# Kernel optimization log

Hardware: AMD Instinct MI355X
Metric: run time of the kernel (lower is better)

## Reference

```python
import jax, jax.numpy as jnp
import numpy as np

WS = 7
C = 384
NH = 12
HD = C // NH
HID = 4 * C


def layernorm(x, g, b, eps=1e-5):
    m = jnp.mean(x, axis=-1, keepdims=True)
    v = jnp.mean((x - m) ** 2, axis=-1, keepdims=True)
    return (x - m) * jax.lax.rsqrt(v + eps) * g + b


def setup_inputs() -> dict:
    key = jax.random.key(0)
    ks = jax.random.split(key, 12)
    s = 0.02
    return {
        "tokens": jax.random.normal(ks[0], (2, 8, 56 * 56, C), jnp.float32),
        "in_proj_w": jax.random.normal(ks[1], (3 * C, C), jnp.float32) * s,
        "in_proj_b": jnp.zeros((3 * C,), jnp.float32),
        "out_w": jax.random.normal(ks[2], (C, C), jnp.float32) * s,
        "out_b": jnp.zeros((C,), jnp.float32),
        "ln1_g": jnp.ones((C,), jnp.float32),
        "ln1_b": jnp.zeros((C,), jnp.float32),
        "w1": jax.random.normal(ks[3], (HID, C), jnp.float32) * s,
        "b1": jnp.zeros((HID,), jnp.float32),
        "w2": jax.random.normal(ks[4], (C, HID), jnp.float32) * s,
        "b2": jnp.zeros((C,), jnp.float32),
        "ln2_g": jnp.ones((C,), jnp.float32),
        "ln2_b": jnp.zeros((C,), jnp.float32),
        "h": 56,
        "w": 56,
    }


def _block(tokens, in_proj_w, in_proj_b, out_w, out_b, ln1_g, ln1_b, w1, b1, w2, b2, ln2_g, ln2_b, h, w):
    b, t, _, c = tokens.shape
    orig_h, orig_w = h, w
    x = tokens.reshape(b, t, h, w, c)
    pad_h = (-h) % WS
    pad_w = (-w) % WS
    if pad_h > 0 or pad_w > 0:
        x = jnp.pad(x, ((0, 0), (0, 0), (0, pad_h), (0, pad_w), (0, 0)))
        h, w = h + pad_h, w + pad_w
    nh, nw = h // WS, w // WS
    # window partition -> [N, 49, C]
    x = x.reshape(b, t, nh, WS, nw, WS, c).transpose(0, 1, 2, 4, 3, 5, 6)
    win = x.reshape(b * t * nh * nw, WS * WS, c)
    # MHA (torch nn.MultiheadAttention semantics)
    a = layernorm(win, ln1_g, ln1_b)
    qkv = a @ in_proj_w.T + in_proj_b  # [N, 49, 3C]
    q, k, v = jnp.split(qkv, 3, axis=-1)
    n, s, _ = q.shape
    q = q.reshape(n, s, NH, HD).transpose(0, 2, 1, 3)
    k = k.reshape(n, s, NH, HD).transpose(0, 2, 1, 3)
    v = v.reshape(n, s, NH, HD).transpose(0, 2, 1, 3)
    scores = jnp.einsum("nhqd,nhkd->nhqk", q, k) / jnp.sqrt(jnp.asarray(HD, q.dtype))
    p = jax.nn.softmax(scores, axis=-1)
    o = jnp.einsum("nhqk,nhkd->nhqd", p, v).transpose(0, 2, 1, 3).reshape(n, s, c)
    win = win + (o @ out_w.T + out_b)
    # MLP
    m = layernorm(win, ln2_g, ln2_b)
    m = jax.nn.gelu(m @ w1.T + b1, approximate=False) @ w2.T + b2
    win = win + m
    # window reverse
    x = win.reshape(b, t, nh, nw, WS, WS, c).transpose(0, 1, 2, 4, 3, 5, 6).reshape(b, t, h, w, c)
    x = x[:, :, :orig_h, :orig_w, :]
    return x.reshape(b, t, orig_h * orig_w, c)


def reference(tokens, in_proj_w, in_proj_b, out_w, out_b, ln1_g, ln1_b, w1, b1, w2, b2, ln2_g, ln2_b, h, w):
    return _block(tokens, in_proj_w, in_proj_b, out_w, out_b, ln1_g, ln1_b, w1, b1, w2, b2, ln2_g, ln2_b, h, w)
```

## Files before the change

kernel.cpp:

```cpp
#include <hip/hip_runtime.h>
#include <hip/hip_bf16.h>
#include <math.h>

using short8 = __attribute__((ext_vector_type(8))) short;
using f32x4  = __attribute__((ext_vector_type(4))) float;

#define MFMA_B16(A,B,C) __builtin_amdgcn_mfma_f32_16x16x32_bf16((A),(B),(C),0,0,0)

#define ALN_STR 392
#define Q2_OFF  38416
#define QK_STR  72
#define K2_OFF  45472
#define VT_OFF  52528
#define VT_STR  72
#define OH_OFF  61744
#define OH_STR  72
#define HID0_OFF 38416
#define HID1_OFF 55824
#define HID_STR 136
#define SMEM_BYTES 80896

__device__ __forceinline__ unsigned f2bf(float x) {
  unsigned u = __float_as_uint(x);
  return (u + 0x7fffu + ((u >> 16) & 1u)) >> 16;
}

template<bool WBF>
__device__ __forceinline__ short8 loadW(const void* base, int tile, int K8, int kcb,
                                        int l, int row, int ldk, int k0) {
  if constexpr (WBF) {
    return *(const short8*)((const unsigned short*)base +
                            (((size_t)(tile * K8 + kcb)) << 7) + l * 8);
  } else {
    const float* p = (const float*)base + (size_t)row * ldk + k0;
    float4 x = *(const float4*)p;
    float4 y = *(const float4*)(p + 4);
    short8 r;
    r[0]=(short)f2bf(x.x); r[1]=(short)f2bf(x.y); r[2]=(short)f2bf(x.z); r[3]=(short)f2bf(x.w);
    r[4]=(short)f2bf(y.x); r[5]=(short)f2bf(y.y); r[6]=(short)f2bf(y.z); r[7]=(short)f2bf(y.w);
    return r;
  }
}

__global__ void cvt_pack(const float* __restrict__ src, unsigned short* __restrict__ dst,
                         int K, int n) {
  int K8 = K >> 3;
  int i = blockIdx.x * blockDim.x + threadIdx.x;
  if (i >= n) return;
  int e = i & 7;
  int idx = i >> 3;
  int r = idx & 15; idx >>= 4;
  int kc = idx % K8, ci = idx / K8;
  dst[i] = (unsigned short)f2bf(src[(size_t)(ci * 16 + r) * K + kc * 8 + e]);
}

template<bool WBF>
__global__ __launch_bounds__(512, 4)
void swin_mfma(const float* __restrict__ tokens,
               const void* __restrict__ ipw,  const float* __restrict__ ipb,
               const void* __restrict__ outw, const float* __restrict__ outb,
               const float* __restrict__ ln1g, const float* __restrict__ ln1b,
               const void* __restrict__ w1,   const float* __restrict__ b1,
               const void* __restrict__ w2,   const float* __restrict__ b2,
               const float* __restrict__ ln2g, const float* __restrict__ ln2b,
               float* __restrict__ out)
{
  extern __shared__ char smem[];
  unsigned short* aln  = (unsigned short*)smem;
  unsigned short* q2   = (unsigned short*)(smem + Q2_OFF);
  unsigned short* k2   = (unsigned short*)(smem + K2_OFF);
  unsigned short* vT2  = (unsigned short*)(smem + VT_OFF);
  unsigned short* oh   = (unsigned short*)(smem + OH_OFF);
  unsigned short* hid0 = (unsigned short*)(smem + HID0_OFF);
  unsigned short* hid1 = (unsigned short*)(smem + HID1_OFF);

  const int tid = threadIdx.x;
  const int l  = tid & 63, wv = tid >> 6;
  const int cl = l & 15,  kg = l >> 4;
  const int wid = blockIdx.x;
  const int iw = wid & 7, ih = (wid >> 3) & 7, bt = wid >> 6;

  auto gidx = [&](int r, int c) -> size_t {
    int wi = r / 7, wj = r - wi * 7;
    return ((size_t)bt * 3136 + (size_t)((ih*7 + wi) * 56 + iw*7 + wj)) * 384 + c;
  };

  auto ln_pass = [&](const float* src, const float* gw, const float* gb) {
    int grp = tid >> 3, lj = tid & 7;
    if (grp < 49) {
      size_t base = gidx(grp, 0);
      float4 xv[12];
      float sx = 0.f, sxx = 0.f;
      #pragma unroll
      for (int k = 0; k < 12; ++k) {
        xv[k] = *(const float4*)&src[base + (lj + 8*k) * 4];
        sx  += xv[k].x + xv[k].y + xv[k].z + xv[k].w;
        sxx += xv[k].x*xv[k].x + xv[k].y*xv[k].y + xv[k].z*xv[k].z + xv[k].w*xv[k].w;
      }
      #pragma unroll
      for (int d = 1; d < 8; d <<= 1) { sx += __shfl_xor(sx, d, 8); sxx += __shfl_xor(sxx, d, 8); }
      float mean = sx * (1.f/384.f);
      float rs = rsqrtf(sxx * (1.f/384.f) - mean*mean + 1e-5f);
      unsigned short* arow = aln + grp * ALN_STR;
      #pragma unroll
      for (int k = 0; k < 12; ++k) {
        int c = (lj + 8*k) * 4;
        float4 gv = *(const float4*)&gw[c];
        float4 bv = *(const float4*)&gb[c];
        unsigned u0 = f2bf((xv[k].x-mean)*rs*gv.x + bv.x) | (f2bf((xv[k].y-mean)*rs*gv.y + bv.y) << 16);
        unsigned u1 = f2bf((xv[k].z-mean)*rs*gv.z + bv.z) | (f2bf((xv[k].w-mean)*rs*gv.w + bv.w) << 16);
        *(uint2*)&arow[c] = make_uint2(u0, u1);
      }
    }
  };

  const int ri0 = wv & 3, chalf = wv >> 2;
  const int arow0 = (cl + 16 * ri0) * ALN_STR;

  auto qkv = [&](int pr) {
    #pragma unroll
    for (int half = 0; half < 2; ++half) {
      int cia[3], tilea[3], growa[3];
      #pragma unroll
      for (int j = 0; j < 3; ++j) {
        int ci = chalf + 2 * (half * 3 + j);
        int part = ci >> 2, wt = ci & 3;
        cia[j] = ci;
        tilea[j] = part * 24 + pr * 4 + wt;
        growa[j] = part * 384 + pr * 64 + wt * 16 + cl;
      }
      f32x4 d0{0,0,0,0}, d1{0,0,0,0}, d2{0,0,0,0};
      #pragma unroll
      for (int kt = 0; kt < 12; ++kt) {
        int k0 = kt * 32 + kg * 8;
        short8 a = *(const short8*)&aln[arow0 + k0];
        short8 b0 = loadW<WBF>(ipw, tilea[0], 48, kt*4, l, growa[0], 384, k0);
        short8 b1 = loadW<WBF>(ipw, tilea[1], 48, kt*4, l, growa[1], 384, k0);
        short8 b2 = loadW<WBF>(ipw, tilea[2], 48, kt*4, l, growa[2], 384, k0);
        d0 = MFMA_B16(a, b0, d0);
        d1 = MFMA_B16(a, b1, d1);
        d2 = MFMA_B16(a, b2, d2);
      }
      #pragma unroll
      for (int j = 0; j < 3; ++j) {
        f32x4 dd = (j == 0) ? d0 : (j == 1) ? d1 : d2;
        int part = cia[j] >> 2;
        int within = (cia[j] & 3) * 16 + cl;
        float bias = ipb[growa[j]];
        float scl = (part == 0) ? 0.17677669529663687f : 1.f;
        #pragma unroll
        for (int rg = 0; rg < 4; ++rg) {
          int row = kg * 4 + rg + 16 * ri0;
          if (row < 49) {
            unsigned short bv = (unsigned short)f2bf((dd[rg] + bias) * scl);
            if      (part == 0) q2[row * QK_STR + within] = bv;
            else if (part == 1) k2[row * QK_STR + within] = bv;
            else                vT2[within * VT_STR + row] = bv;
          }
        }
      }
    }
  };

  for (int i = tid; i < (64*VT_STR)/2; i += 512) ((unsigned*)(smem + VT_OFF))[i] = 0u;
  ln_pass(tokens, ln1g, ln1b);
  __syncthreads();

  f32x4 opacc[3][4];
  #pragma unroll
  for (int a = 0; a < 3; ++a)
    #pragma unroll
    for (int b = 0; b < 4; ++b) opacc[a][b] = f32x4{0.f,0.f,0.f,0.f};

  qkv(0);
  __syncthreads();

  const int hl = wv & 1, qci = wv >> 1;

  for (int pr = 0; pr < 6; ++pr) {
    {
      short8 bq = *(const short8*)&q2[(16*qci + cl) * QK_STR + hl*32 + kg*8];
      f32x4 dsc[4];
      #pragma unroll
      for (int kri = 0; kri < 4; ++kri) {
        short8 ak = *(const short8*)&k2[(16*kri + cl) * QK_STR + hl*32 + kg*8];
        f32x4 z{0.f,0.f,0.f,0.f};
        dsc[kri] = MFMA_B16(ak, bq, z);
      }
      float ev[4][4];
      float mx = -1e30f;
      #pragma unroll
      for (int kri = 0; kri < 4; ++kri)
        #pragma unroll
        for (int r = 0; r < 4; ++r) {
          int kidx = 16*kri + 4*kg + r;
          float v = (kidx < 49) ? dsc[kri][r] : -1e30f;
          ev[kri][r] = v;
          mx = fmaxf(mx, v);
        }
      mx = fmaxf(mx, __shfl_xor(mx, 16));
      mx = fmaxf(mx, __shfl_xor(mx, 32));
      float sum = 0.f;
      #pragma unroll
      for (int kri = 0; kri < 4; ++kri)
        #pragma unroll
        for (int r = 0; r < 4; ++r) {
          float e = __expf(ev[kri][r] - mx);
          ev[kri][r] = e; sum += e;
        }
      sum += __shfl_xor(sum, 16);
      sum += __shfl_xor(sum, 32);
      float inv = 1.f / sum;
      unsigned pk[4][2];
      #pragma unroll
      for (int kri = 0; kri < 4; ++kri) {
        pk[kri][0] = f2bf(ev[kri][0]*inv) | (f2bf(ev[kri][1]*inv) << 16);
        pk[kri][1] = f2bf(ev[kri][2]*inv) | (f2bf(ev[kri][3]*inv) << 16);
      }
      f32x4 dot0{0.f,0.f,0.f,0.f}, dot1{0.f,0.f,0.f,0.f};
      const int sA = cl + 32 * (kg & 1);
      const bool hi = (kg >> 1) & 1;
      #pragma unroll
      for (int kt = 0; kt < 2; ++kt) {
        unsigned x0 = (unsigned)__shfl((int)pk[2*kt][0],   sA);
        unsigned x1 = (unsigned)__shfl((int)pk[2*kt][1],   sA);
        unsigned x2 = (unsigned)__shfl((int)pk[2*kt][0],   sA + 16);
        unsigned x3 = (unsigned)__shfl((int)pk[2*kt][1],   sA + 16);
        unsigned y0 = (unsigned)__shfl((int)pk[2*kt+1][0], sA);
        unsigned y1 = (unsigned)__shfl((int)pk[2*kt+1][1], sA);
        unsigned y2 = (unsigned)__shfl((int)pk[2*kt+1][0], sA + 16);
        unsigned y3 = (unsigned)__shfl((int)pk[2*kt+1][1], sA + 16);
        uint4 bu = make_uint4(hi ? y0 : x0, hi ? y1 : x1, hi ? y2 : x2, hi ? y3 : x3);
        short8 bfrag = *(short8*)&bu;
        short8 a0 = *(const short8*)&vT2[(hl*32 +  0 + cl) * VT_STR + kt*32 + kg*8];
        short8 a1 = *(const short8*)&vT2[(hl*32 + 16 + cl) * VT_STR + kt*32 + kg*8];
        dot0 = MFMA_B16(a0, bfrag, dot0);
        dot1 = MFMA_B16(a1, bfrag, dot1);
      }
      int q = 16*qci + cl;
      if (q < 49) {
        int base = q * OH_STR + hl*32 + kg*4;
        *(unsigned*)&oh[base     ] = f2bf(dot0[0]) | (f2bf(dot0[1]) << 16);
        *(unsigned*)&oh[base +  2] = f2bf(dot0[2]) | (f2bf(dot0[3]) << 16);
        *(unsigned*)&oh[base + 16] = f2bf(dot1[0]) | (f2bf(dot1[1]) << 16);
        *(unsigned*)&oh[base + 18] = f2bf(dot1[2]) | (f2bf(dot1[3]) << 16);
      }
    }
    __syncthreads();

    {
      short8 ao[4][2];
      #pragma unroll
      for (int ri = 0; ri < 4; ++ri)
        #pragma unroll
        for (int kt = 0; kt < 2; ++kt)
          ao[ri][kt] = *(const short8*)&oh[(cl + 16*ri) * OH_STR + kt*32 + kg*8];
      #pragma unroll
      for (int cii = 0; cii < 3; ++cii) {
        #pragma unroll
        for (int kt = 0; kt < 2; ++kt) {
          short8 bw = loadW<WBF>(outw, wv*3 + cii, 48, pr*8 + kt*4, l,
                                 (wv*3 + cii)*16 + cl, 384, pr*64 + kt*32 + kg*8);
          opacc[cii][0] = MFMA_B16(ao[0][kt], bw, opacc[cii][0]);
          opacc[cii][1] = MFMA_B16(ao[1][kt], bw, opacc[cii][1]);
          opacc[cii][2] = MFMA_B16(ao[2][kt], bw, opacc[cii][2]);
          opacc[cii][3] = MFMA_B16(ao[3][kt], bw, opacc[cii][3]);
        }
      }
      if (pr < 5) qkv(pr + 1);
    }
    __syncthreads();
  }

  #pragma unroll
  for (int cii = 0; cii < 3; ++cii) {
    int col = (wv*3 + cii) * 16 + cl;
    float ob = outb[col];
    #pragma unroll
    for (int ri = 0; ri < 4; ++ri) {
      #pragma unroll
      for (int rg = 0; rg < 4; ++rg) {
        int row = kg*4 + rg + 16*ri;
        if (row < 49) {
          size_t g = gidx(row, col);
          out[g] = tokens[g] + opacc[cii][ri][rg] + ob;
        }
      }
    }
  }
  __syncthreads();

  ln_pass(out, ln2g, ln2b);
  __syncthreads();

  f32x4 macc[3][4];
  #pragma unroll
  for (int a = 0; a < 3; ++a)
    #pragma unroll
    for (int b = 0; b < 4; ++b) macc[a][b] = f32x4{0.f,0.f,0.f,0.f};

  auto mlp1 = [&](int cc, unsigned short* hb) {
    int tile = cc * 8 + wv;
    int n = cc * 128 + wv * 16 + cl;
    f32x4 e0{0,0,0,0}, e1{0,0,0,0}, e2{0,0,0,0}, e3{0,0,0,0};
    #pragma unroll
    for (int kt = 0; kt < 12; ++kt) {
      int k0 = kt * 32 + kg * 8;
      short8 bw = loadW<WBF>(w1, tile, 48, kt*4, l, n, 384, k0);
      short8 a0 = *(const short8*)&aln[(cl     ) * ALN_STR + k0];
      short8 a1 = *(const short8*)&aln[(cl + 16) * ALN_STR + k0];
      short8 a2 = *(const short8*)&aln[(cl + 32) * ALN_STR + k0];
      short8 a3 = *(const short8*)&aln[(cl + 48) * ALN_STR + k0];
      e0 = MFMA_B16(a0, bw, e0);
      e1 = MFMA_B16(a1, bw, e1);
      e2 = MFMA_B16(a2, bw, e2);
      e3 = MFMA_B16(a3, bw, e3);
    }
    float bb = b1[n];
    #pragma unroll
    for (int ri = 0; ri < 4; ++ri) {
      f32x4 ee = (ri == 0) ? e0 : (ri == 1) ? e1 : (ri == 2) ? e2 : e3;
      #pragma unroll
      for (int rg = 0; rg < 4; ++rg) {
        int row = kg*4 + rg + 16*ri;
        if (row < 49) {
          float x = ee[rg] + bb;
          float gl = 0.5f * x * (1.f + erff(x * 0.70710678118654752f));
          hb[row * HID_STR + wv*16 + cl] = (unsigned short)f2bf(gl);
        }
      }
    }
  };
  auto mlp2 = [&](int cc, const unsigned short* hb) {
    #pragma unroll
    for (int kt = 0; kt < 4; ++kt) {
      int k0 = kt * 32 + kg * 8;
      short8 h0_ = *(const short8*)&hb[(cl     ) * HID_STR + k0];
      short8 h1_ = *(const short8*)&hb[(cl + 16) * HID_STR + k0];
      short8 h2_ = *(const short8*)&hb[(cl + 32) * HID_STR + k0];
      short8 h3_ = *(const short8*)&hb[(cl + 48) * HID_STR + k0];
      #pragma unroll
      for (int cii = 0; cii < 3; ++cii) {
        short8 bw = loadW<WBF>(w2, wv*3 + cii, 192, cc*16 + kt*4, l,
                               (wv*3 + cii)*16 + cl, 1536, cc*128 + k0);
        macc[cii][0] = MFMA_B16(h0_, bw, macc[cii][0]);
        macc[cii][1] = MFMA_B16(h1_, bw, macc[cii][1]);
        macc[cii][2] = MFMA_B16(h2_, bw, macc[cii][2]);
        macc[cii][3] = MFMA_B16(h3_, bw, macc[cii][3]);
      }
    }
  };

  mlp1(0, hid0);
  __syncthreads();
  for (int cc = 1; cc < 12; ++cc) {
    mlp2(cc - 1, ((cc - 1) & 1) ? hid1 : hid0);
    mlp1(cc, (cc & 1) ? hid1 : hid0);
    __syncthreads();
  }
  mlp2(11, hid1);

  #pragma unroll
  for (int cii = 0; cii < 3; ++cii) {
    int col = (wv*3 + cii) * 16 + cl;
    float bb2 = b2[col];
    #pragma unroll
    for (int ri = 0; ri < 4; ++ri) {
      #pragma unroll
      for (int rg = 0; rg < 4; ++rg) {
        int row = kg*4 + rg + 16*ri;
        if (row < 49) {
          size_t g = gidx(row, col);
          out[g] = out[g] + macc[cii][ri][rg] + bb2;
        }
      }
    }
  }
}

#define WS_IPW  0
#define WS_OUTW 442368
#define WS_W1   589824
#define WS_W2   1179648
#define WS_TOT  1769472

extern "C" void kernel_launch(void* const* d_in, const int* in_sizes, int n_in,
                              void* d_out, int out_size, void* d_ws, size_t ws_size,
                              hipStream_t stream) {
  (void)in_sizes; (void)n_in; (void)out_size;
  const float* tokens = (const float*)d_in[0];
  const float* ipw  = (const float*)d_in[1];
  const float* ipb  = (const float*)d_in[2];
  const float* outw = (const float*)d_in[3];
  const float* outb = (const float*)d_in[4];
  const float* ln1g = (const float*)d_in[5];
  const float* ln1b = (const float*)d_in[6];
  const float* w1   = (const float*)d_in[7];
  const float* b1   = (const float*)d_in[8];
  const float* w2   = (const float*)d_in[9];
  const float* b2   = (const float*)d_in[10];
  const float* ln2g = (const float*)d_in[11];
  const float* ln2b = (const float*)d_in[12];
  float* out = (float*)d_out;

  bool wbf = (ws_size >= (size_t)WS_TOT * 2);
  if (wbf) {
    unsigned short* wsp = (unsigned short*)d_ws;
    hipLaunchKernelGGL(cvt_pack, dim3((442368+511)/512), dim3(512), 0, stream, ipw,  wsp + WS_IPW,  384,  442368);
    hipLaunchKernelGGL(cvt_pack, dim3((147456+511)/512), dim3(512), 0, stream, outw, wsp + WS_OUTW, 384,  147456);
    hipLaunchKernelGGL(cvt_pack, dim3((589824+511)/512), dim3(512), 0, stream, w1,   wsp + WS_W1,   384,  589824);
    hipLaunchKernelGGL(cvt_pack, dim3((589824+511)/512), dim3(512), 0, stream, w2,   wsp + WS_W2,   1536, 589824);
    (void)hipFuncSetAttribute((const void*)swin_mfma<true>,
                              hipFuncAttributeMaxDynamicSharedMemorySize, SMEM_BYTES);
    hipLaunchKernelGGL((swin_mfma<true>), dim3(1024), dim3(512), SMEM_BYTES, stream,
                       tokens, (const void*)(wsp + WS_IPW), ipb,
                       (const void*)(wsp + WS_OUTW), outb, ln1g, ln1b,
                       (const void*)(wsp + WS_W1), b1, (const void*)(wsp + WS_W2), b2,
                       ln2g, ln2b, out);
  } else {
    (void)hipFuncSetAttribute((const void*)swin_mfma<false>,
                              hipFuncAttributeMaxDynamicSharedMemorySize, SMEM_BYTES);
    hipLaunchKernelGGL((swin_mfma<false>), dim3(1024), dim3(512), SMEM_BYTES, stream,
                       tokens, (const void*)ipw, ipb, (const void*)outw, outb, ln1g, ln1b,
                       (const void*)w1, b1, (const void*)w2, b2, ln2g, ln2b, out);
  }
}
```

Baseline: 475.2 us.

## Process two windows per 1024-thread block, prefetch weights, use tanh-form GELU

Each block now holds two 49-token windows with 1024 threads, each with its own LDS region, so the block count is halved. The QKV, MLP1 and MLP2 loops now load the next k-step's weight fragments into registers before issuing the current MFMAs, to hide global-load latency. The exact erf GELU is replaced by a tanh approximation written as x*sigmoid, which is cheaper but changes numerics slightly. Using 146 KB of LDS per block caps residency at one block per CU, and the extra prefetch registers may spill.

```diff
diff --git a/kernel.cpp b/kernel.cpp
--- a/kernel.cpp
+++ b/kernel.cpp
@@ -8,21 +8,21 @@
 #define MFMA_B16(A,B,C) __builtin_amdgcn_mfma_f32_16x16x32_bf16((A),(B),(C),0,0,0)
 
 #define ALN_STR 392
-#define Q2_OFF  38416
+#define ALN_SZ  38416
+#define POOL    76832
+#define PS      34816
 #define QK_STR  72
-#define K2_OFF  45472
-#define VT_OFF  52528
 #define VT_STR  72
-#define OH_OFF  61744
 #define OH_STR  72
-#define HID0_OFF 38416
-#define HID1_OFF 55824
 #define HID_STR 136
-#define SMEM_BYTES 80896
-
-__device__ __forceinline__ unsigned f2bf(float x) {
+#define SMEM_BYTES 146464
+
+__device__ __forceinline__ unsigned short f2bfu(float x) {
   unsigned u = __float_as_uint(x);
-  return (u + 0x7fffu + ((u >> 16) & 1u)) >> 16;
+  return (unsigned short)((u + 0x7fffu + ((u >> 16) & 1u)) >> 16);
+}
+__device__ __forceinline__ unsigned pk2(float a, float b) {
+  return (unsigned)f2bfu(a) | ((unsigned)f2bfu(b) << 16);
 }
 
 template<bool WBF>
@@ -36,8 +36,8 @@
     float4 x = *(const float4*)p;
     float4 y = *(const float4*)(p + 4);
     short8 r;
-    r[0]=(short)f2bf(x.x); r[1]=(short)f2bf(x.y); r[2]=(short)f2bf(x.z); r[3]=(short)f2bf(x.w);
-    r[4]=(short)f2bf(y.x); r[5]=(short)f2bf(y.y); r[6]=(short)f2bf(y.z); r[7]=(short)f2bf(y.w);
+    r[0]=(short)f2bfu(x.x); r[1]=(short)f2bfu(x.y); r[2]=(short)f2bfu(x.z); r[3]=(short)f2bfu(x.w);
+    r[4]=(short)f2bfu(y.x); r[5]=(short)f2bfu(y.y); r[6]=(short)f2bfu(y.z); r[7]=(short)f2bfu(y.w);
     return r;
   }
 }
@@ -51,11 +51,11 @@
   int idx = i >> 3;
   int r = idx & 15; idx >>= 4;
   int kc = idx % K8, ci = idx / K8;
-  dst[i] = (unsigned short)f2bf(src[(size_t)(ci * 16 + r) * K + kc * 8 + e]);
+  dst[i] = f2bfu(src[(size_t)(ci * 16 + r) * K + kc * 8 + e]);
 }
 
 template<bool WBF>
-__global__ __launch_bounds__(512, 4)
+__global__ __launch_bounds__(1024, 4)
 void swin_mfma(const float* __restrict__ tokens,
                const void* __restrict__ ipw,  const float* __restrict__ ipb,
                const void* __restrict__ outw, const float* __restrict__ outb,
@@ -66,19 +66,22 @@
                float* __restrict__ out)
 {
   extern __shared__ char smem[];
-  unsigned short* aln  = (unsigned short*)smem;
-  unsigned short* q2   = (unsigned short*)(smem + Q2_OFF);
-  unsigned short* k2   = (unsigned short*)(smem + K2_OFF);
-  unsigned short* vT2  = (unsigned short*)(smem + VT_OFF);
-  unsigned short* oh   = (unsigned short*)(smem + OH_OFF);
-  unsigned short* hid0 = (unsigned short*)(smem + HID0_OFF);
-  unsigned short* hid1 = (unsigned short*)(smem + HID1_OFF);
-
   const int tid = threadIdx.x;
-  const int l  = tid & 63, wv = tid >> 6;
-  const int cl = l & 15,  kg = l >> 4;
-  const int wid = blockIdx.x;
+  const int win = tid >> 9;
+  const int wv  = (tid >> 6) & 7;
+  const int l   = tid & 63;
+  const int cl  = l & 15, kg = l >> 4;
+  const int wid = blockIdx.x * 2 + win;
   const int iw = wid & 7, ih = (wid >> 3) & 7, bt = wid >> 6;
+
+  unsigned short* aln = (unsigned short*)(smem + win * ALN_SZ);
+  char* pool = smem + POOL + win * PS;
+  unsigned short* q2   = (unsigned short*)(pool);
+  unsigned short* k2   = (unsigned short*)(pool + 7056);
+  unsigned short* vT2  = (unsigned short*)(pool + 14112);
+  unsigned short* oh   = (unsigned short*)(pool + 23328);
+  unsigned short* hid0 = (unsigned short*)(pool);
+  unsigned short* hid1 = (unsigned short*)(pool + 17408);
 
   auto gidx = [&](int r, int c) -> size_t {
     int wi = r / 7, wj = r - wi * 7;
@@ -86,9 +89,9 @@
   };
 
   auto ln_pass = [&](const float* src, const float* gw, const float* gb) {
-    int grp = tid >> 3, lj = tid & 7;
-    if (grp < 49) {
-      size_t base = gidx(grp, 0);
+    int row = (tid >> 3) & 63, lj = tid & 7;
+    if (row < 49) {
+      size_t base = gidx(row, 0);
       float4 xv[12];
       float sx = 0.f, sxx = 0.f;
       #pragma unroll
@@ -101,14 +104,14 @@
       for (int d = 1; d < 8; d <<= 1) { sx += __shfl_xor(sx, d, 8); sxx += __shfl_xor(sxx, d, 8); }
       float mean = sx * (1.f/384.f);
       float rs = rsqrtf(sxx * (1.f/384.f) - mean*mean + 1e-5f);
-      unsigned short* arow = aln + grp * ALN_STR;
+      unsigned short* arow = aln + row * ALN_STR;
       #pragma unroll
       for (int k = 0; k < 12; ++k) {
         int c = (lj + 8*k) * 4;
         float4 gv = *(const float4*)&gw[c];
         float4 bv = *(const float4*)&gb[c];
-        unsigned u0 = f2bf((xv[k].x-mean)*rs*gv.x + bv.x) | (f2bf((xv[k].y-mean)*rs*gv.y + bv.y) << 16);
-        unsigned u1 = f2bf((xv[k].z-mean)*rs*gv.z + bv.z) | (f2bf((xv[k].w-mean)*rs*gv.w + bv.w) << 16);
+        unsigned u0 = pk2((xv[k].x-mean)*rs*gv.x + bv.x, (xv[k].y-mean)*rs*gv.y + bv.y);
+        unsigned u1 = pk2((xv[k].z-mean)*rs*gv.z + bv.z, (xv[k].w-mean)*rs*gv.w + bv.w);
         *(uint2*)&arow[c] = make_uint2(u0, u1);
       }
     }
@@ -120,49 +123,56 @@
   auto qkv = [&](int pr) {
     #pragma unroll
     for (int half = 0; half < 2; ++half) {
-      int cia[3], tilea[3], growa[3];
+      int tilea[3], growa[3], parta[3], wta[3];
       #pragma unroll
       for (int j = 0; j < 3; ++j) {
         int ci = chalf + 2 * (half * 3 + j);
-        int part = ci >> 2, wt = ci & 3;
-        cia[j] = ci;
-        tilea[j] = part * 24 + pr * 4 + wt;
-        growa[j] = part * 384 + pr * 64 + wt * 16 + cl;
+        parta[j] = ci >> 2; wta[j] = ci & 3;
+        tilea[j] = parta[j] * 24 + pr * 4 + wta[j];
+        growa[j] = parta[j] * 384 + pr * 64 + wta[j] * 16 + cl;
       }
       f32x4 d0{0,0,0,0}, d1{0,0,0,0}, d2{0,0,0,0};
+      short8 a_c  = *(const short8*)&aln[arow0 + kg*8];
+      short8 b0_c = loadW<WBF>(ipw, tilea[0], 48, 0, l, growa[0], 384, kg*8);
+      short8 b1_c = loadW<WBF>(ipw, tilea[1], 48, 0, l, growa[1], 384, kg*8);
+      short8 b2_c = loadW<WBF>(ipw, tilea[2], 48, 0, l, growa[2], 384, kg*8);
       #pragma unroll
       for (int kt = 0; kt < 12; ++kt) {
-        int k0 = kt * 32 + kg * 8;
-        short8 a = *(const short8*)&aln[arow0 + k0];
-        short8 b0 = loadW<WBF>(ipw, tilea[0], 48, kt*4, l, growa[0], 384, k0);
-        short8 b1 = loadW<WBF>(ipw, tilea[1], 48, kt*4, l, growa[1], 384, k0);
-        short8 b2 = loadW<WBF>(ipw, tilea[2], 48, kt*4, l, growa[2], 384, k0);
-        d0 = MFMA_B16(a, b0, d0);
-        d1 = MFMA_B16(a, b1, d1);
-        d2 = MFMA_B16(a, b2, d2);
+        short8 a_n, b0_n, b1_n, b2_n;
+        if (kt < 11) {
+          int k1 = (kt+1)*32 + kg*8;
+          a_n  = *(const short8*)&aln[arow0 + k1];
+          b0_n = loadW<WBF>(ipw, tilea[0], 48, (kt+1)*4, l, growa[0], 384, k1);
+          b1_n = loadW<WBF>(ipw, tilea[1], 48, (kt+1)*4, l, growa[1], 384, k1);
+          b2_n = loadW<WBF>(ipw, tilea[2], 48, (kt+1)*4, l, growa[2], 384, k1);
+        }
+        d0 = MFMA_B16(a_c, b0_c, d0);
+        d1 = MFMA_B16(a_c, b1_c, d1);
+        d2 = MFMA_B16(a_c, b2_c, d2);
+        a_c = a_n; b0_c = b0_n; b1_c = b1_n; b2_c = b2_n;
       }
       #pragma unroll
       for (int j = 0; j < 3; ++j) {
         f32x4 dd = (j == 0) ? d0 : (j == 1) ? d1 : d2;
-        int part = cia[j] >> 2;
-        int within = (cia[j] & 3) * 16 + cl;
+        int within = wta[j] * 16 + cl;
         float bias = ipb[growa[j]];
-        float scl = (part == 0) ? 0.17677669529663687f : 1.f;
+        float scl = (parta[j] == 0) ? 0.17677669529663687f : 1.f;
         #pragma unroll
         for (int rg = 0; rg < 4; ++rg) {
           int row = kg * 4 + rg + 16 * ri0;
           if (row < 49) {
-            unsigned short bv = (unsigned short)f2bf((dd[rg] + bias) * scl);
-            if      (part == 0) q2[row * QK_STR + within] = bv;
-            else if (part == 1) k2[row * QK_STR + within] = bv;
-            else                vT2[within * VT_STR + row] = bv;
+            unsigned short bv = f2bfu((dd[rg] + bias) * scl);
+            if      (parta[j] == 0) q2[row * QK_STR + within] = bv;
+            else if (parta[j] == 1) k2[row * QK_STR + within] = bv;
+            else                    vT2[within * VT_STR + row] = bv;
           }
         }
       }
     }
   };
 
-  for (int i = tid; i < (64*VT_STR)/2; i += 512) ((unsigned*)(smem + VT_OFF))[i] = 0u;
+  for (int i = (tid & 511); i < (64*VT_STR)/2; i += 512)
+    ((unsigned*)(pool + 14112))[i] = 0u;
   ln_pass(tokens, ln1g, ln1b);
   __syncthreads();
 
@@ -214,8 +224,8 @@
       unsigned pk[4][2];
       #pragma unroll
       for (int kri = 0; kri < 4; ++kri) {
-        pk[kri][0] = f2bf(ev[kri][0]*inv) | (f2bf(ev[kri][1]*inv) << 16);
-        pk[kri][1] = f2bf(ev[kri][2]*inv) | (f2bf(ev[kri][3]*inv) << 16);
+        pk[kri][0] = pk2(ev[kri][0]*inv, ev[kri][1]*inv);
+        pk[kri][1] = pk2(ev[kri][2]*inv, ev[kri][3]*inv);
       }
       f32x4 dot0{0.f,0.f,0.f,0.f}, dot1{0.f,0.f,0.f,0.f};
       const int sA = cl + 32 * (kg & 1);
@@ -240,10 +250,10 @@
       int q = 16*qci + cl;
       if (q < 49) {
         int base = q * OH_STR + hl*32 + kg*4;
-        *(unsigned*)&oh[base     ] = f2bf(dot0[0]) | (f2bf(dot0[1]) << 16);
-        *(unsigned*)&oh[base +  2] = f2bf(dot0[2]) | (f2bf(dot0[3]) << 16);
-        *(unsigned*)&oh[base + 16] = f2bf(dot1[0]) | (f2bf(dot1[1]) << 16);
-        *(unsigned*)&oh[base + 18] = f2bf(dot1[2]) | (f2bf(dot1[3]) << 16);
+        *(unsigned*)&oh[base     ] = pk2(dot0[0], dot0[1]);
+        *(unsigned*)&oh[base +  2] = pk2(dot0[2], dot0[3]);
+        *(unsigned*)&oh[base + 16] = pk2(dot1[0], dot1[1]);
+        *(unsigned*)&oh[base + 18] = pk2(dot1[2], dot1[3]);
       }
     }
     __syncthreads();
@@ -303,18 +313,22 @@
     int tile = cc * 8 + wv;
     int n = cc * 128 + wv * 16 + cl;
     f32x4 e0{0,0,0,0}, e1{0,0,0,0}, e2{0,0,0,0}, e3{0,0,0,0};
+    short8 bw_c = loadW<WBF>(w1, tile, 48, 0, l, n, 384, kg*8);
     #pragma unroll
     for (int kt = 0; kt < 12; ++kt) {
+      short8 bw_n;
+      if (kt < 11)
+        bw_n = loadW<WBF>(w1, tile, 48, (kt+1)*4, l, n, 384, (kt+1)*32 + kg*8);
       int k0 = kt * 32 + kg * 8;
-      short8 bw = loadW<WBF>(w1, tile, 48, kt*4, l, n, 384, k0);
       short8 a0 = *(const short8*)&aln[(cl     ) * ALN_STR + k0];
       short8 a1 = *(const short8*)&aln[(cl + 16) * ALN_STR + k0];
       short8 a2 = *(const short8*)&aln[(cl + 32) * ALN_STR + k0];
       short8 a3 = *(const short8*)&aln[(cl + 48) * ALN_STR + k0];
-      e0 = MFMA_B16(a0, bw, e0);
-      e1 = MFMA_B16(a1, bw, e1);
-      e2 = MFMA_B16(a2, bw, e2);
-      e3 = MFMA_B16(a3, bw, e3);
+      e0 = MFMA_B16(a0, bw_c, e0);
+      e1 = MFMA_B16(a1, bw_c, e1);
+      e2 = MFMA_B16(a2, bw_c, e2);
+      e3 = MFMA_B16(a3, bw_c, e3);
+      bw_c = bw_n;
     }
     float bb = b1[n];
     #pragma unroll
@@ -325,29 +339,46 @@
         int row = kg*4 + rg + 16*ri;
         if (row < 49) {
           float x = ee[rg] + bb;
-          float gl = 0.5f * x * (1.f + erff(x * 0.70710678118654752f));
-          hb[row * HID_STR + wv*16 + cl] = (unsigned short)f2bf(gl);
+          float t2 = 0.044715f * x * x;
+          float arg = __builtin_fmaf(t2, x, x);
+          float e = __expf(1.5957691216f * arg);
+          float gl = x * (e / (e + 1.f));
+          hb[row * HID_STR + wv*16 + cl] = f2bfu(gl);
         }
       }
     }
   };
   auto mlp2 = [&](int cc, const unsigned short* hb) {
+    short8 c0_c = loadW<WBF>(w2, wv*3+0, 192, cc*16, l, (wv*3+0)*16+cl, 1536, cc*128 + kg*8);
+    short8 c1_c = loadW<WBF>(w2, wv*3+1, 192, cc*16, l, (wv*3+1)*16+cl, 1536, cc*128 + kg*8);
+    short8 c2_c = loadW<WBF>(w2, wv*3+2, 192, cc*16, l, (wv*3+2)*16+cl, 1536, cc*128 + kg*8);
     #pragma unroll
     for (int kt = 0; kt < 4; ++kt) {
+      short8 c0_n, c1_n, c2_n;
+      if (kt < 3) {
+        int kcb = cc*16 + (kt+1)*4, k1 = cc*128 + (kt+1)*32 + kg*8;
+        c0_n = loadW<WBF>(w2, wv*3+0, 192, kcb, l, (wv*3+0)*16+cl, 1536, k1);
+        c1_n = loadW<WBF>(w2, wv*3+1, 192, kcb, l, (wv*3+1)*16+cl, 1536, k1);
+        c2_n = loadW<WBF>(w2, wv*3+2, 192, kcb, l, (wv*3+2)*16+cl, 1536, k1);
+      }
       int k0 = kt * 32 + kg * 8;
       short8 h0_ = *(const short8*)&hb[(cl     ) * HID_STR + k0];
       short8 h1_ = *(const short8*)&hb[(cl + 16) * HID_STR + k0];
       short8 h2_ = *(const short8*)&hb[(cl + 32) * HID_STR + k0];
       short8 h3_ = *(const short8*)&hb[(cl + 48) * HID_STR + k0];
-      #pragma unroll
-      for (int cii = 0; cii < 3; ++cii) {
-        short8 bw = loadW<WBF>(w2, wv*3 + cii, 192, cc*16 + kt*4, l,
-                               (wv*3 + cii)*16 + cl, 1536, cc*128 + k0);
-        macc[cii][0] = MFMA_B16(h0_, bw, macc[cii][0]);
-        macc[cii][1] = MFMA_B16(h1_, bw, macc[cii][1]);
-        macc[cii][2] = MFMA_B16(h2_, bw, macc[cii][2]);
-        macc[cii][3] = MFMA_B16(h3_, bw, macc[cii][3]);
-      }
+      macc[0][0] = MFMA_B16(h0_, c0_c, macc[0][0]);
+      macc[0][1] = MFMA_B16(h1_, c0_c, macc[0][1]);
+      macc[0][2] = MFMA_B16(h2_, c0_c, macc[0][2]);
+      macc[0][3] = MFMA_B16(h3_, c0_c, macc[0][3]);
+      macc[1][0] = MFMA_B16(h0_, c1_c, macc[1][0]);
+      macc[1][1] = MFMA_B16(h1_, c1_c, macc[1][1]);
+      macc[1][2] = MFMA_B16(h2_, c1_c, macc[1][2]);
+      macc[1][3] = MFMA_B16(h3_, c1_c, macc[1][3]);
+      macc[2][0] = MFMA_B16(h0_, c2_c, macc[2][0]);
+      macc[2][1] = MFMA_B16(h1_, c2_c, macc[2][1]);
+      macc[2][2] = MFMA_B16(h2_, c2_c, macc[2][2]);
+      macc[2][3] = MFMA_B16(h3_, c2_c, macc[2][3]);
+      c0_c = c0_n; c1_c = c1_n; c2_c = c2_n;
     }
   };
 
@@ -412,7 +443,7 @@
     hipLaunchKernelGGL(cvt_pack, dim3((589824+511)/512), dim3(512), 0, stream, w2,   wsp + WS_W2,   1536, 589824);
     (void)hipFuncSetAttribute((const void*)swin_mfma<true>,
                               hipFuncAttributeMaxDynamicSharedMemorySize, SMEM_BYTES);
-    hipLaunchKernelGGL((swin_mfma<true>), dim3(1024), dim3(512), SMEM_BYTES, stream,
+    hipLaunchKernelGGL((swin_mfma<true>), dim3(512), dim3(1024), SMEM_BYTES, stream,
                        tokens, (const void*)(wsp + WS_IPW), ipb,
                        (const void*)(wsp + WS_OUTW), outb, ln1g, ln1b,
                        (const void*)(wsp + WS_W1), b1, (const void*)(wsp + WS_W2), b2,
@@ -420,7 +451,7 @@
   } else {
     (void)hipFuncSetAttribute((const void*)swin_mfma<false>,
                               hipFuncAttributeMaxDynamicSharedMemorySize, SMEM_BYTES);
-    hipLaunchKernelGGL((swin_mfma<false>), dim3(1024), dim3(512), SMEM_BYTES, stream,
+    hipLaunchKernelGGL((swin_mfma<false>), dim3(512), dim3(1024), SMEM_BYTES, stream,
                        tokens, (const void*)ipw, ipb, (const void*)outw, outb, ln1g, ln1b,
                        (const void*)w1, b1, (const void*)w2, b2, ln2g, ln2b, out);
   }
```

New measurement: 501.2 us. 5.5% more time.
